# Kernel optimization log

Measured on AMD Instinct MI355X. Metric: run time of the kernel, lower is better.

Reference implementation:

```python
import jax, jax.numpy as jnp
import numpy as np

S = 4  # MC samples


def _gat_layer(x, mask, w, a_src, a_dst, bias):
    # x: (b,n,fin)  w: (H,fin,fout)  mask: (b,n,n) bool
    h = jnp.einsum('bnf,hfo->bhno', x, w)                      # (b,H,n,fout)
    th = jnp.tanh(h)
    att_src = jnp.einsum('bhno,ho->bhn', th, a_src)
    att_dst = jnp.einsum('bhno,ho->bhn', th, a_dst)
    logits = jax.nn.leaky_relu(att_src[:, :, :, None] + att_dst[:, :, None, :], 0.2)
    logits = jnp.where(mask[:, None, :, :], logits, jnp.float32(-1e9))
    att = jax.nn.softmax(logits, axis=-1)                      # (b,H,n,n)
    out = jnp.einsum('bhij,bhjo->bhio', att, h) + bias         # (b,H,n,fout)
    return out, att


def setup_inputs() -> dict:
    key = jax.random.key(0)
    ks = jax.random.split(key, 11)
    b, n, f0, emb_d = 128, 128, 64, 64
    H1, f1, H2, f2 = 8, 16, 1, 2
    fin1 = f0 + emb_d            # 128 (n_units[0] += 64)
    fin2 = H1 * f1               # 128 (heads concatenated between layers)
    x = jax.random.normal(ks[0], (b, n, f0), jnp.float32)
    emb = jax.random.normal(ks[1], (b, n, emb_d), jnp.float32)
    adj = jax.random.randint(ks[2], (b, n, n), 0, 2).astype(jnp.int32)
    adj = jnp.maximum(adj, jnp.eye(n, dtype=jnp.int32)[None])  # self-loops keep softmax rows valid
    w1 = jax.random.normal(ks[3], (S, H1, fin1, f1), jnp.float32) * 0.1
    a_src1 = jax.random.normal(ks[4], (S, H1, f1), jnp.float32) * 0.1
    a_dst1 = jax.random.normal(ks[5], (S, H1, f1), jnp.float32) * 0.1
    b1 = jax.random.normal(ks[6], (f1,), jnp.float32) * 0.1
    w2 = jax.random.normal(ks[7], (S, H2, fin2, f2), jnp.float32) * 0.1
    a_src2 = jax.random.normal(ks[8], (S, H2, f2), jnp.float32) * 0.1
    a_dst2 = jax.random.normal(ks[9], (S, H2, f2), jnp.float32) * 0.1
    b2 = jax.random.normal(ks[10], (f2,), jnp.float32) * 0.1
    return dict(x=x, emb=emb, adj=adj, w1=w1, a_src1=a_src1, a_dst1=a_dst1, b1=b1,
                w2=w2, a_src2=a_src2, a_dst2=a_dst2, b2=b2)


def reference(x, emb, adj, w1, a_src1, a_dst1, b1, w2, a_src2, a_dst2, b2):
    mask = adj.astype(bool)
    x0 = jnp.concatenate([x, emb], axis=-1)                    # (b,n,128)
    b, n = x0.shape[0], x0.shape[1]
    xs = jnp.broadcast_to(x0, (S,) + x0.shape)                 # same input for each MC sample
    layer = jax.vmap(_gat_layer, in_axes=(0, None, 0, 0, 0, None))
    # layer 1 (per-sample variational weights), ELU activation
    h1, att1 = layer(xs, mask, w1, a_src1, a_dst1, b1)         # h1: (S,b,H1,n,f1)
    h1 = jax.nn.elu(h1)
    # concat heads: transpose(1,2).view(bs,n,-1)
    xs2 = jnp.transpose(h1, (0, 1, 3, 2, 4)).reshape(S, b, n, -1)
    # layer 2 (last layer): no activation, mean over heads
    h2, att2 = layer(xs2, mask, w2, a_src2, a_dst2, b2)        # (S,b,1,n,2)
    out = h2.mean(axis=2)                                      # (S,b,n,2)
    logp = jax.nn.log_softmax(out, axis=-1)[:, :, -1, :]       # (S,b,2) -> ego node
    result = jnp.mean(logp, axis=0)                            # var_mean -> mean (return_uncertainty=False)
    return result
```

## Files before the change

### kernel.cpp

```cpp
#include <hip/hip_runtime.h>
#include <stdint.h>
#include <math.h>

typedef __attribute__((ext_vector_type(8))) short short8;
typedef __attribute__((ext_vector_type(4))) float floatx4;

#define L_HF    0
#define L_H2P   32768
#define L_SRC   40960
#define L_DST   45056
#define L_MASK  49152
#define L_RED   51200
#define L_D2    51456
#define L_SIZE  51968

#define WS_MASK_BYTES 262144
#define WS_W1F_BYTES  131072

union F8 { short8 s8; uint32_t u[4]; };

__device__ __forceinline__ uint32_t packbf(float a, float b){
  uint32_t ua = __float_as_uint(a), ub = __float_as_uint(b);
  uint32_t ra = (ua + 0x7fffu + ((ua>>16)&1u)) >> 16;
  uint32_t rb = (ub + 0x7fffu + ((ub>>16)&1u)) >> 16;
  return ra | (rb<<16);
}
__device__ __forceinline__ float fast_tanh(float x){
  float e = __expf(2.f*x);
  return 1.f - 2.f*__builtin_amdgcn_rcpf(e + 1.f);
}

__global__ void prep(const int* __restrict__ adj, const float* __restrict__ w1,
                     uint32_t* __restrict__ mask_ws, uint32_t* __restrict__ w1f) {
  const int blk = blockIdx.x, t = threadIdx.x;
  if (blk < 1024) {
    const int lane = t & 63;
    const int row0 = blk*16 + (t>>6)*4;
    #pragma unroll
    for (int i=0;i<4;++i){
      const int row = row0 + i;
      const int* ar = adj + (size_t)row*128;
      uint64_t m0 = __ballot(ar[lane] != 0);
      uint64_t m1 = __ballot(ar[64+lane] != 0);
      if (lane == 0)
        ((uint4*)mask_ws)[row] = make_uint4((uint32_t)m0,(uint32_t)(m0>>32),
                                            (uint32_t)m1,(uint32_t)(m1>>32));
    }
  } else {
    const int tid = (blk-1024)*256 + t;
    const int lane = tid & 63, ks = (tid>>6)&3, ct = (tid>>8)&7, s = tid>>11;
    const float* wp = w1 + s*16384 + ct*2048 + (ks*32 + (lane>>4)*8)*16 + (lane&15);
    uint4 u;
    u.x = packbf(wp[0*16],  wp[1*16]);
    u.y = packbf(wp[2*16],  wp[3*16]);
    u.z = packbf(wp[4*16],  wp[5*16]);
    u.w = packbf(wp[6*16],  wp[7*16]);
    ((uint4*)w1f)[tid] = u;
  }
}

__global__ __launch_bounds__(512,4) void gat_fused(
    const float* __restrict__ x,  const float* __restrict__ emb,
    const float* __restrict__ a_src1, const float* __restrict__ a_dst1,
    const float* __restrict__ b1,
    const float* __restrict__ w2, const float* __restrict__ a_src2,
    const float* __restrict__ a_dst2, const float* __restrict__ b2,
    const uint32_t* __restrict__ mask_ws, const char* __restrict__ w1f,
    float* __restrict__ outp)
{
  __shared__ __align__(16) char smem[L_SIZE];
  char*     hf    = smem + L_HF;
  uint32_t* hf_u  = (uint32_t*)(smem + L_HF);
  float2*   h2p   = (float2*)(smem + L_H2P);
  float*    src_l = (float*)(smem + L_SRC);
  float*    dst_l = (float*)(smem + L_DST);
  uint32_t* mask_l= (uint32_t*)(smem + L_MASK);
  const uint4* mask4 = (const uint4*)(smem + L_MASK);
  float*    red   = (float*)(smem + L_RED);
  float*    d2_l  = (float*)(smem + L_D2);

  const int t  = threadIdx.x;
  const int s  = blockIdx.x >> 7;
  const int bb = blockIdx.x & 127;
  const int lane = t & 63, w = t >> 6;
  const int of = lane & 15, kg = lane >> 4;

  mask_l[t] = mask_ws[(size_t)bb*512 + t];

  const int arow = w*16 + of;
  const float* xrow = x   + ((size_t)bb*128 + arow)*64;
  const float* erow = emb + ((size_t)bb*128 + arow)*64;
  short8 af[4];
  #pragma unroll
  for (int ks=0; ks<4; ++ks){
    int k = ks*32 + kg*8;
    const float* p = (k<64) ? (xrow+k) : (erow + (k-64));
    float4 f0 = *(const float4*)p, f1 = *(const float4*)(p+4);
    F8 fr;
    fr.u[0]=packbf(f0.x,f0.y); fr.u[1]=packbf(f0.z,f0.w);
    fr.u[2]=packbf(f1.x,f1.y); fr.u[3]=packbf(f1.z,f1.w);
    af[ks]=fr.s8;
  }

  const char* w1fs = w1f + (size_t)s*32768;
  floatx4 acc[8];
  #pragma unroll
  for (int ct=0; ct<8; ++ct) acc[ct]=(floatx4){0.f,0.f,0.f,0.f};
  #pragma unroll
  for (int ct=0; ct<8; ++ct)
    #pragma unroll
    for (int ks=0; ks<4; ++ks){
      short8 bfr = *(const short8*)(w1fs + ((ct*4+ks)*64 + lane)*16);
      acc[ct] = __builtin_amdgcn_mfma_f32_16x16x32_bf16(af[ks], bfr, acc[ct], 0,0,0);
    }

  const int ks_h = w>>1, kgp = (w&1)*2 + (kg>>1), vv = (kg&1)*2;
  #pragma unroll
  for (int ct=0; ct<8; ++ct){
    float asv = a_src1[s*128 + ct*16 + of];
    float adv = a_dst1[s*128 + ct*16 + of];
    float ps[4], pd[4];
    #pragma unroll
    for (int r=0; r<4; ++r){
      float th = fast_tanh(acc[ct][r]);
      ps[r] = th*asv; pd[r] = th*adv;
    }
    #pragma unroll
    for (int off=1; off<16; off<<=1)
      #pragma unroll
      for (int r=0; r<4; ++r){ ps[r]+=__shfl_xor(ps[r],off); pd[r]+=__shfl_xor(pd[r],off); }
    if (of==0){
      #pragma unroll
      for (int r=0; r<4; ++r){
        int i = w*16 + kg*4 + r;
        src_l[ct*128+i]=ps[r]; dst_l[ct*128+i]=pd[r];
      }
    }
    uint32_t p0 = packbf(acc[ct][0], acc[ct][1]);
    uint32_t p1 = packbf(acc[ct][2], acc[ct][3]);
    uint32_t* dsth = hf_u + ((ct*4+ks_h)*64 + kgp*16 + of)*4 + vv;
    *(uint2*)dsth = make_uint2(p0, p1);
  }
  __syncthreads();

  const int hd = w;
  float b1v  = b1[of];
  float w2c0 = w2[s*256 + (hd*16+of)*2 + 0];
  float w2c1 = w2[s*256 + (hd*16+of)*2 + 1];
  short8 hb[4];
  #pragma unroll
  for (int ks=0; ks<4; ++ks)
    hb[ks] = *(const short8*)(hf + ((hd*4+ks)*64 + lane)*16);

  for (int rt=0; rt<8; ++rt){
    const int im = rt*16 + of;
    float srcv = src_l[hd*128 + im];
    uint4 mrow = mask4[im];
    floatx4 acc2 = (floatx4){0.f,0.f,0.f,0.f};
    float zp = 0.f;
    #pragma unroll
    for (int ks=0; ks<4; ++ks){
      const float* dp = dst_l + hd*128 + ks*32 + kg*8;
      float4 d0 = *(const float4*)dp, d1 = *(const float4*)(dp+4);
      uint32_t mw = (ks==0)?mrow.x:(ks==1)?mrow.y:(ks==2)?mrow.z:mrow.w;
      uint32_t mbyte = mw >> (kg*8);
      float dj[8] = {d0.x,d0.y,d0.z,d0.w,d1.x,d1.y,d1.z,d1.w};
      float e[8];
      #pragma unroll
      for (int jj=0; jj<8; ++jj){
        float t0 = srcv + dj[jj];
        float lr = fmaxf(t0, 0.2f*t0);
        float ev = __expf(lr);
        ev = ((mbyte>>jj)&1u) ? ev : 0.f;
        e[jj]=ev; zp += ev;
      }
      F8 fr;
      fr.u[0]=packbf(e[0],e[1]); fr.u[1]=packbf(e[2],e[3]);
      fr.u[2]=packbf(e[4],e[5]); fr.u[3]=packbf(e[6],e[7]);
      acc2 = __builtin_amdgcn_mfma_f32_16x16x32_bf16(fr.s8, hb[ks], acc2, 0,0,0);
    }
    float zr = zp + __shfl_xor(zp,16); zr += __shfl_xor(zr,32);
    float zi = __builtin_amdgcn_rcpf(zr);
    float pc0[4], pc1[4];
    #pragma unroll
    for (int r=0; r<4; ++r){
      float ziR = __shfl(zi, kg*4+r);
      float o  = fmaf(acc2[r], ziR, b1v);
      float oe = (o>0.f) ? o : (__expf(o)-1.f);
      pc0[r]=oe*w2c0; pc1[r]=oe*w2c1;
    }
    #pragma unroll
    for (int off=1; off<16; off<<=1)
      #pragma unroll
      for (int r=0; r<4; ++r){ pc0[r]+=__shfl_xor(pc0[r],off); pc1[r]+=__shfl_xor(pc1[r],off); }
    if (of==0){
      #pragma unroll
      for (int r=0; r<4; ++r){
        int i = rt*16 + kg*4 + r;
        h2p[w*128 + i] = make_float2(pc0[r], pc1[r]);
      }
    }
  }
  __syncthreads();

  {
    const int jn = t>>1, cc = t&1;
    const bool act = (t<256);
    float hv=0.f, v=-1e9f;
    if (act){
      #pragma unroll
      for (int ww=0; ww<8; ++ww){
        float2 p = h2p[ww*128+jn];
        hv += cc ? p.y : p.x;
      }
      float th2 = fast_tanh(hv);
      float ps2 = th2*a_src2[s*2+cc];
      float pd2 = th2*a_dst2[s*2+cc];
      ps2 += __shfl_xor(ps2,1);
      pd2 += __shfl_xor(pd2,1);
      if (cc==0) d2_l[jn]=pd2;
      if (t==254) red[40]=ps2;
    }
    __syncthreads();
    if (act){
      float t0 = red[40] + d2_l[jn];
      float lg = fmaxf(t0, 0.2f*t0);
      uint32_t bit = (mask_l[127*4 + (jn>>5)] >> (jn&31)) & 1u;
      v = bit ? lg : -1e9f;
    }
    float mloc = v;
    #pragma unroll
    for (int off=32; off>=1; off>>=1) mloc = fmaxf(mloc, __shfl_xor(mloc,off));
    if (lane==0) red[w]=mloc;
    __syncthreads();
    float M = fmaxf(fmaxf(red[0],red[1]), fmaxf(red[2],red[3]));
    float e2 = act ? __expf(v-M) : 0.f;
    float vA = e2*hv;
    float vZ = (cc==0 && act) ? e2 : 0.f;
    #pragma unroll
    for (int off=2; off<=32; off<<=1){ vA+=__shfl_xor(vA,off); vZ+=__shfl_xor(vZ,off); }
    if (lane==0){ red[8+w]=vA; red[24+w]=vZ; }
    if (lane==1){ red[16+w]=vA; }
    __syncthreads();
    if (t==0){
      float S0 = red[8]+red[9]+red[10]+red[11];
      float S1 = red[16]+red[17]+red[18]+red[19];
      float Z  = red[24]+red[25]+red[26]+red[27];
      float o0 = S0/Z + b2[0];
      float o1 = S1/Z + b2[1];
      float mm = fmaxf(o0,o1);
      float lse = mm + logf(__expf(o0-mm)+__expf(o1-mm));
      atomicAdd(outp + bb*2 + 0, 0.25f*(o0 - lse));
      atomicAdd(outp + bb*2 + 1, 0.25f*(o1 - lse));
    }
  }
}

extern "C" void kernel_launch(void* const* d_in, const int* in_sizes, int n_in,
                              void* d_out, int out_size, void* d_ws, size_t ws_size,
                              hipStream_t stream) {
  const float* x      = (const float*)d_in[0];
  const float* emb    = (const float*)d_in[1];
  const int*   adj    = (const int*)d_in[2];
  const float* w1     = (const float*)d_in[3];
  const float* a_src1 = (const float*)d_in[4];
  const float* a_dst1 = (const float*)d_in[5];
  const float* b1     = (const float*)d_in[6];
  const float* w2     = (const float*)d_in[7];
  const float* a_src2 = (const float*)d_in[8];
  const float* a_dst2 = (const float*)d_in[9];
  const float* b2     = (const float*)d_in[10];

  uint32_t* mask_ws = (uint32_t*)d_ws;
  uint32_t* w1f     = (uint32_t*)((char*)d_ws + WS_MASK_BYTES);

  hipMemsetAsync(d_out, 0, (size_t)out_size*sizeof(float), stream);
  prep<<<dim3(1056), dim3(256), 0, stream>>>(adj, w1, mask_ws, w1f);
  gat_fused<<<dim3(512), dim3(512), 0, stream>>>(x, emb, a_src1, a_dst1, b1,
                                                 w2, a_src2, a_dst2, b2,
                                                 mask_ws, (const char*)w1f,
                                                 (float*)d_out);
}
```

Before: 139.8 us.

## Split heads across two blocks, fold prep into main kernel, add tail kernel

Removes the separate prep kernel and memset. Each block now builds its adjacency bitmask and its slice of bf16 w1 fragments in shared memory. Work per (sample, batch) is split into two blocks of four heads each, which halves the shared-memory footprint and raises the occupancy target, while all 8 waves run the attention loop. A new small tail kernel sums the partial layer-2 features from a workspace and does the final softmax and averaging without atomics. It also switches to exp2 with pre-scaled coefficients and truncating bf16 packing for the attention weights, at the cost of redundant mask building per block and a slight precision change.

Result: no change. 139.0 us (-0.6%).

```diff
diff --git a/kernel.cpp b/kernel.cpp
--- a/kernel.cpp
+++ b/kernel.cpp
@@ -6,18 +6,20 @@
 typedef __attribute__((ext_vector_type(4))) float floatx4;
 
 #define L_HF    0
-#define L_H2P   32768
-#define L_SRC   40960
-#define L_DST   45056
-#define L_MASK  49152
-#define L_RED   51200
-#define L_D2    51456
-#define L_SIZE  51968
-
-#define WS_MASK_BYTES 262144
-#define WS_W1F_BYTES  131072
+#define L_SRC   16384
+#define L_DST   18432
+#define L_MASK  20480
+#define L_H2P   22528
+#define L_SIZE  26624
 
 union F8 { short8 s8; uint32_t u[4]; };
+
+#if __has_builtin(__builtin_amdgcn_exp2f)
+#define EXP2F __builtin_amdgcn_exp2f
+#else
+#define EXP2F exp2f
+#endif
+#define LOG2E 1.4426950408889634f
 
 __device__ __forceinline__ uint32_t packbf(float a, float b){
   uint32_t ua = __float_as_uint(a), ub = __float_as_uint(b);
@@ -25,67 +27,37 @@
   uint32_t rb = (ub + 0x7fffu + ((ub>>16)&1u)) >> 16;
   return ra | (rb<<16);
 }
+__device__ __forceinline__ uint32_t packbf_t(float a, float b){
+  return __builtin_amdgcn_perm(__float_as_uint(b), __float_as_uint(a), 0x07060302u);
+}
 __device__ __forceinline__ float fast_tanh(float x){
   float e = __expf(2.f*x);
   return 1.f - 2.f*__builtin_amdgcn_rcpf(e + 1.f);
 }
 
-__global__ void prep(const int* __restrict__ adj, const float* __restrict__ w1,
-                     uint32_t* __restrict__ mask_ws, uint32_t* __restrict__ w1f) {
-  const int blk = blockIdx.x, t = threadIdx.x;
-  if (blk < 1024) {
-    const int lane = t & 63;
-    const int row0 = blk*16 + (t>>6)*4;
-    #pragma unroll
-    for (int i=0;i<4;++i){
-      const int row = row0 + i;
-      const int* ar = adj + (size_t)row*128;
-      uint64_t m0 = __ballot(ar[lane] != 0);
-      uint64_t m1 = __ballot(ar[64+lane] != 0);
-      if (lane == 0)
-        ((uint4*)mask_ws)[row] = make_uint4((uint32_t)m0,(uint32_t)(m0>>32),
-                                            (uint32_t)m1,(uint32_t)(m1>>32));
-    }
-  } else {
-    const int tid = (blk-1024)*256 + t;
-    const int lane = tid & 63, ks = (tid>>6)&3, ct = (tid>>8)&7, s = tid>>11;
-    const float* wp = w1 + s*16384 + ct*2048 + (ks*32 + (lane>>4)*8)*16 + (lane&15);
-    uint4 u;
-    u.x = packbf(wp[0*16],  wp[1*16]);
-    u.y = packbf(wp[2*16],  wp[3*16]);
-    u.z = packbf(wp[4*16],  wp[5*16]);
-    u.w = packbf(wp[6*16],  wp[7*16]);
-    ((uint4*)w1f)[tid] = u;
-  }
-}
-
-__global__ __launch_bounds__(512,4) void gat_fused(
+__global__ __launch_bounds__(512,8) void gat_fused(
     const float* __restrict__ x,  const float* __restrict__ emb,
+    const int* __restrict__ adj,  const float* __restrict__ w1,
     const float* __restrict__ a_src1, const float* __restrict__ a_dst1,
-    const float* __restrict__ b1,
-    const float* __restrict__ w2, const float* __restrict__ a_src2,
-    const float* __restrict__ a_dst2, const float* __restrict__ b2,
-    const uint32_t* __restrict__ mask_ws, const char* __restrict__ w1f,
-    float* __restrict__ outp)
+    const float* __restrict__ b1, const float* __restrict__ w2,
+    float* __restrict__ ws_h2)
 {
   __shared__ __align__(16) char smem[L_SIZE];
   char*     hf    = smem + L_HF;
   uint32_t* hf_u  = (uint32_t*)(smem + L_HF);
-  float2*   h2p   = (float2*)(smem + L_H2P);
   float*    src_l = (float*)(smem + L_SRC);
   float*    dst_l = (float*)(smem + L_DST);
   uint32_t* mask_l= (uint32_t*)(smem + L_MASK);
   const uint4* mask4 = (const uint4*)(smem + L_MASK);
-  float*    red   = (float*)(smem + L_RED);
-  float*    d2_l  = (float*)(smem + L_D2);
-
-  const int t  = threadIdx.x;
-  const int s  = blockIdx.x >> 7;
-  const int bb = blockIdx.x & 127;
+  float2*   h2p   = (float2*)(smem + L_H2P);
+
+  const int t    = threadIdx.x;
+  const int blk  = blockIdx.x;
+  const int s    = blk >> 8;
+  const int bb   = (blk & 255) >> 1;
+  const int half = blk & 1;
   const int lane = t & 63, w = t >> 6;
   const int of = lane & 15, kg = lane >> 4;
-
-  mask_l[t] = mask_ws[(size_t)bb*512 + t];
 
   const int arow = w*16 + of;
   const float* xrow = x   + ((size_t)bb*128 + arow)*64;
@@ -102,23 +74,55 @@
     af[ks]=fr.s8;
   }
 
-  const char* w1fs = w1f + (size_t)s*32768;
-  floatx4 acc[8];
-  #pragma unroll
-  for (int ct=0; ct<8; ++ct) acc[ct]=(floatx4){0.f,0.f,0.f,0.f};
-  #pragma unroll
-  for (int ct=0; ct<8; ++ct)
+  {
+    const float* w1s = w1 + (size_t)s*16384 + half*8192;
+    #pragma unroll
+    for (int r=0; r<2; ++r){
+      int q = t + r*512;
+      int ql = q & 63, ks = (q>>6)&3, ct = q>>8;
+      const float* wp = w1s + ct*2048 + (ks*32 + (ql>>4)*8)*16 + (ql&15);
+      F8 fr;
+      fr.u[0]=packbf(wp[0],  wp[16]);
+      fr.u[1]=packbf(wp[32], wp[48]);
+      fr.u[2]=packbf(wp[64], wp[80]);
+      fr.u[3]=packbf(wp[96], wp[112]);
+      *(short8*)(hf + ((ct*4+ks)*64 + ql)*16) = fr.s8;
+    }
+  }
+
+  {
+    const int* adjb = adj + (size_t)bb*16384;
+    #pragma unroll 4
+    for (int rr=0; rr<16; ++rr){
+      const int row = w*16 + rr;
+      const int* ar = adjb + row*128;
+      uint64_t m0 = __ballot(ar[lane] != 0);
+      uint64_t m1 = __ballot(ar[64+lane] != 0);
+      if (lane == 0)
+        ((uint4*)mask_l)[row] = make_uint4((uint32_t)m0,(uint32_t)(m0>>32),
+                                           (uint32_t)m1,(uint32_t)(m1>>32));
+    }
+  }
+  __syncthreads();
+
+  floatx4 acc[4];
+  #pragma unroll
+  for (int ct=0; ct<4; ++ct) acc[ct]=(floatx4){0.f,0.f,0.f,0.f};
+  #pragma unroll
+  for (int ct=0; ct<4; ++ct)
     #pragma unroll
     for (int ks=0; ks<4; ++ks){
-      short8 bfr = *(const short8*)(w1fs + ((ct*4+ks)*64 + lane)*16);
+      short8 bfr = *(const short8*)(hf + ((ct*4+ks)*64 + lane)*16);
       acc[ct] = __builtin_amdgcn_mfma_f32_16x16x32_bf16(af[ks], bfr, acc[ct], 0,0,0);
     }
+  __syncthreads();
 
   const int ks_h = w>>1, kgp = (w&1)*2 + (kg>>1), vv = (kg&1)*2;
   #pragma unroll
-  for (int ct=0; ct<8; ++ct){
-    float asv = a_src1[s*128 + ct*16 + of];
-    float adv = a_dst1[s*128 + ct*16 + of];
+  for (int ct=0; ct<4; ++ct){
+    const int ghd = half*4 + ct;
+    float asv = a_src1[s*128 + ghd*16 + of] * LOG2E;
+    float adv = a_dst1[s*128 + ghd*16 + of] * LOG2E;
     float ps[4], pd[4];
     #pragma unroll
     for (int r=0; r<4; ++r){
@@ -143,24 +147,27 @@
   }
   __syncthreads();
 
-  const int hd = w;
+  const int lhd = w >> 1;
+  const int ghd = half*4 + lhd;
   float b1v  = b1[of];
-  float w2c0 = w2[s*256 + (hd*16+of)*2 + 0];
-  float w2c1 = w2[s*256 + (hd*16+of)*2 + 1];
+  float w2c0 = w2[s*256 + (ghd*16+of)*2 + 0];
+  float w2c1 = w2[s*256 + (ghd*16+of)*2 + 1];
   short8 hb[4];
   #pragma unroll
   for (int ks=0; ks<4; ++ks)
-    hb[ks] = *(const short8*)(hf + ((hd*4+ks)*64 + lane)*16);
-
-  for (int rt=0; rt<8; ++rt){
+    hb[ks] = *(const short8*)(hf + ((lhd*4+ks)*64 + lane)*16);
+
+  #pragma unroll
+  for (int rtl=0; rtl<4; ++rtl){
+    const int rt = (w&1)*4 + rtl;
     const int im = rt*16 + of;
-    float srcv = src_l[hd*128 + im];
+    float srcv = src_l[lhd*128 + im];
     uint4 mrow = mask4[im];
     floatx4 acc2 = (floatx4){0.f,0.f,0.f,0.f};
     float zp = 0.f;
     #pragma unroll
     for (int ks=0; ks<4; ++ks){
-      const float* dp = dst_l + hd*128 + ks*32 + kg*8;
+      const float* dp = dst_l + lhd*128 + ks*32 + kg*8;
       float4 d0 = *(const float4*)dp, d1 = *(const float4*)(dp+4);
       uint32_t mw = (ks==0)?mrow.x:(ks==1)?mrow.y:(ks==2)?mrow.z:mrow.w;
       uint32_t mbyte = mw >> (kg*8);
@@ -170,13 +177,13 @@
       for (int jj=0; jj<8; ++jj){
         float t0 = srcv + dj[jj];
         float lr = fmaxf(t0, 0.2f*t0);
-        float ev = __expf(lr);
+        float ev = EXP2F(lr);
         ev = ((mbyte>>jj)&1u) ? ev : 0.f;
         e[jj]=ev; zp += ev;
       }
       F8 fr;
-      fr.u[0]=packbf(e[0],e[1]); fr.u[1]=packbf(e[2],e[3]);
-      fr.u[2]=packbf(e[4],e[5]); fr.u[3]=packbf(e[6],e[7]);
+      fr.u[0]=packbf_t(e[0],e[1]); fr.u[1]=packbf_t(e[2],e[3]);
+      fr.u[2]=packbf_t(e[4],e[5]); fr.u[3]=packbf_t(e[6],e[7]);
       acc2 = __builtin_amdgcn_mfma_f32_16x16x32_bf16(fr.s8, hb[ks], acc2, 0,0,0);
     }
     float zr = zp + __shfl_xor(zp,16); zr += __shfl_xor(zr,32);
@@ -197,63 +204,78 @@
       #pragma unroll
       for (int r=0; r<4; ++r){
         int i = rt*16 + kg*4 + r;
-        h2p[w*128 + i] = make_float2(pc0[r], pc1[r]);
+        h2p[lhd*128 + i] = make_float2(pc0[r], pc1[r]);
       }
     }
   }
   __syncthreads();
 
-  {
+  if (t < 256){
     const int jn = t>>1, cc = t&1;
-    const bool act = (t<256);
-    float hv=0.f, v=-1e9f;
-    if (act){
-      #pragma unroll
-      for (int ww=0; ww<8; ++ww){
-        float2 p = h2p[ww*128+jn];
-        hv += cc ? p.y : p.x;
-      }
-      float th2 = fast_tanh(hv);
-      float ps2 = th2*a_src2[s*2+cc];
-      float pd2 = th2*a_dst2[s*2+cc];
-      ps2 += __shfl_xor(ps2,1);
-      pd2 += __shfl_xor(pd2,1);
-      if (cc==0) d2_l[jn]=pd2;
-      if (t==254) red[40]=ps2;
-    }
+    float hv = 0.f;
+    #pragma unroll
+    for (int hd2=0; hd2<4; ++hd2){
+      float2 p = h2p[hd2*128+jn];
+      hv += cc ? p.y : p.x;
+    }
+    ws_h2[(size_t)blk*256 + t] = hv;
+  }
+}
+
+__global__ __launch_bounds__(256) void gat_tail(
+    const float* __restrict__ ws_h2, const int* __restrict__ adj,
+    const float* __restrict__ a_src2, const float* __restrict__ a_dst2,
+    const float* __restrict__ b2, float* __restrict__ out)
+{
+  __shared__ float d2_l[128];
+  __shared__ float red[16];
+  __shared__ float srcE;
+  const int bb = blockIdx.x, t = threadIdx.x;
+  const int jn = t>>1, cc = t&1, lane = t&63, w = t>>6;
+  const uint32_t bit = (adj[((size_t)bb*128+127)*128 + jn] != 0) ? 1u : 0u;
+  float acc0=0.f, acc1=0.f;
+  for (int s=0; s<4; ++s){
+    float hv = ws_h2[(size_t)(s*256 + bb*2 + 0)*256 + t]
+             + ws_h2[(size_t)(s*256 + bb*2 + 1)*256 + t];
+    float th2 = fast_tanh(hv);
+    float ps2 = th2*a_src2[s*2+cc];
+    float pd2 = th2*a_dst2[s*2+cc];
+    ps2 += __shfl_xor(ps2,1);
+    pd2 += __shfl_xor(pd2,1);
+    if (s) __syncthreads();
+    if (cc==0) d2_l[jn]=pd2;
+    if (t==254) srcE=ps2;
     __syncthreads();
-    if (act){
-      float t0 = red[40] + d2_l[jn];
-      float lg = fmaxf(t0, 0.2f*t0);
-      uint32_t bit = (mask_l[127*4 + (jn>>5)] >> (jn&31)) & 1u;
-      v = bit ? lg : -1e9f;
-    }
+    float t0 = srcE + d2_l[jn];
+    float lg = fmaxf(t0, 0.2f*t0);
+    float v  = bit ? lg : -1e9f;
     float mloc = v;
     #pragma unroll
     for (int off=32; off>=1; off>>=1) mloc = fmaxf(mloc, __shfl_xor(mloc,off));
     if (lane==0) red[w]=mloc;
     __syncthreads();
     float M = fmaxf(fmaxf(red[0],red[1]), fmaxf(red[2],red[3]));
-    float e2 = act ? __expf(v-M) : 0.f;
+    float e2 = __expf(v-M);
     float vA = e2*hv;
-    float vZ = (cc==0 && act) ? e2 : 0.f;
+    float vZ = (cc==0) ? e2 : 0.f;
     #pragma unroll
     for (int off=2; off<=32; off<<=1){ vA+=__shfl_xor(vA,off); vZ+=__shfl_xor(vZ,off); }
-    if (lane==0){ red[8+w]=vA; red[24+w]=vZ; }
-    if (lane==1){ red[16+w]=vA; }
+    if (lane==0){ red[4+w]=vA; red[12+w]=vZ; }
+    if (lane==1){ red[8+w]=vA; }
     __syncthreads();
     if (t==0){
-      float S0 = red[8]+red[9]+red[10]+red[11];
-      float S1 = red[16]+red[17]+red[18]+red[19];
-      float Z  = red[24]+red[25]+red[26]+red[27];
+      float S0 = red[4]+red[5]+red[6]+red[7];
+      float S1 = red[8]+red[9]+red[10]+red[11];
+      float Z  = red[12]+red[13]+red[14]+red[15];
       float o0 = S0/Z + b2[0];
       float o1 = S1/Z + b2[1];
       float mm = fmaxf(o0,o1);
       float lse = mm + logf(__expf(o0-mm)+__expf(o1-mm));
-      atomicAdd(outp + bb*2 + 0, 0.25f*(o0 - lse));
-      atomicAdd(outp + bb*2 + 1, 0.25f*(o1 - lse));
-    }
-  }
+      acc0 += 0.25f*(o0 - lse);
+      acc1 += 0.25f*(o1 - lse);
+    }
+  }
+  if (t==0){ out[bb*2+0]=acc0; out[bb*2+1]=acc1; }
 }
 
 extern "C" void kernel_launch(void* const* d_in, const int* in_sizes, int n_in,
@@ -271,13 +293,10 @@
   const float* a_dst2 = (const float*)d_in[9];
   const float* b2     = (const float*)d_in[10];
 
-  uint32_t* mask_ws = (uint32_t*)d_ws;
-  uint32_t* w1f     = (uint32_t*)((char*)d_ws + WS_MASK_BYTES);
-
-  hipMemsetAsync(d_out, 0, (size_t)out_size*sizeof(float), stream);
-  prep<<<dim3(1056), dim3(256), 0, stream>>>(adj, w1, mask_ws, w1f);
-  gat_fused<<<dim3(512), dim3(512), 0, stream>>>(x, emb, a_src1, a_dst1, b1,
-                                                 w2, a_src2, a_dst2, b2,
-                                                 mask_ws, (const char*)w1f,
-                                                 (float*)d_out);
-}
+  float* ws_h2 = (float*)d_ws;
+
+  gat_fused<<<dim3(1024), dim3(512), 0, stream>>>(x, emb, adj, w1, a_src1, a_dst1,
+                                                  b1, w2, ws_h2);
+  gat_tail<<<dim3(128), dim3(256), 0, stream>>>(ws_h2, adj, a_src2, a_dst2, b2,
+                                                (float*)d_out);
+}
```
